# Optimization experiments

Hardware: AMD Instinct MI355X
Metric: run time of the kernel (lower is better)

## Reference

```python
import jax, jax.numpy as jnp
import numpy as np

NUM_HEADS = 16
ROPE_BASE = 10000.0
NEG_INF = float('-inf')


def _rotate_half_interleaved(x):
    # x: [..., d]; interleaved rotation: (-x2, x1) pairs
    x1 = x[..., ::2]
    x2 = x[..., 1::2]
    return jnp.stack((-x2, x1), axis=-1).reshape(x.shape)


def _rope_tables(seq_len, head_dim, dtype):
    inv_freq = 1.0 / (ROPE_BASE ** (jnp.arange(0, head_dim, 2, dtype=jnp.float32) / head_dim))
    pos = jnp.arange(seq_len, dtype=jnp.float32)
    freqs = pos[:, None] * inv_freq[None, :]          # [S, d/2]
    emb = jnp.concatenate((freqs, freqs), axis=-1)    # [S, d]  (HF-style concat, as in source)
    return jnp.cos(emb).astype(dtype), jnp.sin(emb).astype(dtype)


def setup_inputs() -> dict:
    key = jax.random.key(0)
    ks = jax.random.split(key, 4)
    B, S, H = 2, 2048, 2048
    scale = 0.02
    x = jax.random.normal(ks[0], (B, S, H), dtype=jnp.float32)
    qkv_w = jax.random.normal(ks[1], (3 * H, H), dtype=jnp.float32) * scale
    qkv_b = jnp.zeros((3 * H,), dtype=jnp.float32)
    out_w = jax.random.normal(ks[2], (H, H), dtype=jnp.float32) * scale
    out_b = jnp.zeros((H,), dtype=jnp.float32)
    attention_mask = jnp.ones((B, S), dtype=jnp.int32)
    return {"x": x, "attention_mask": attention_mask, "qkv_w": qkv_w,
            "qkv_b": qkv_b, "out_w": out_w, "out_b": out_b}


def reference(x, attention_mask, qkv_w, qkv_b, out_w, out_b):
    B, S, H = x.shape
    nh = NUM_HEADS
    hd = H // nh
    scale = hd ** -0.5

    qkv = x @ qkv_w.T + qkv_b                            # [B,S,3H]
    qkv = qkv.reshape(B, S, 3, nh, hd).transpose(2, 0, 3, 1, 4)  # [3,B,nh,S,hd]
    q, k, v = qkv[0], qkv[1], qkv[2]

    cos, sin = _rope_tables(S, hd, x.dtype)              # [S,hd]
    cos = cos[None, None, :, :]
    sin = sin[None, None, :, :]
    q = q * cos + _rotate_half_interleaved(q) * sin
    k = k * cos + _rotate_half_interleaved(k) * sin

    scores = jnp.einsum('bhqd,bhkd->bhqk', q, k) * scale  # [B,nh,S,S]
    causal = jnp.triu(jnp.ones((S, S), dtype=bool), k=1)
    scores = jnp.where(causal[None, None], NEG_INF, scores)
    key_mask = (attention_mask == 0)[:, None, None, :]    # [B,1,1,S]
    scores = jnp.where(key_mask, NEG_INF, scores)

    weights = jax.nn.softmax(scores, axis=-1)
    attn = jnp.einsum('bhqk,bhkd->bhqd', weights, v)       # [B,nh,S,hd]
    attn = attn.transpose(0, 2, 1, 3).reshape(B, S, H)
    return attn @ out_w.T + out_b
```

## Files before the change

### kernel.cpp

```cpp
#include <hip/hip_runtime.h>

typedef __bf16 bf16;
typedef __bf16 bf16x4 __attribute__((ext_vector_type(4)));
typedef __bf16 bf16x8 __attribute__((ext_vector_type(8)));
typedef float f32x4 __attribute__((ext_vector_type(4)));

#define MFMA_BF16(a, b, c) __builtin_amdgcn_mfma_f32_16x16x32_bf16(a, b, c, 0, 0, 0)

__device__ __forceinline__ void async16(const void* g, void* l) {
    __builtin_amdgcn_global_load_lds(
        (const __attribute__((address_space(1))) void*)g,
        (__attribute__((address_space(3))) void*)l,
        16, 0, 0);
}

__global__ void cvt8(const float* __restrict__ in, bf16* __restrict__ out, int n) {
    int i = (blockIdx.x * 256 + threadIdx.x) * 8;
    if (i >= n) return;
    float4 a = *(const float4*)(in + i);
    float4 b = *(const float4*)(in + i + 4);
    bf16x8 o;
    o[0] = (bf16)a.x; o[1] = (bf16)a.y; o[2] = (bf16)a.z; o[3] = (bf16)a.w;
    o[4] = (bf16)b.x; o[5] = (bf16)b.y; o[6] = (bf16)b.z; o[7] = (bf16)b.w;
    *(bf16x8*)(out + i) = o;
}

__global__ void tables_k(const int* __restrict__ am, float* __restrict__ cosT,
                         float* __restrict__ sinT, float* __restrict__ mbias) {
    int i = blockIdx.x * 256 + threadIdx.x;
    int s = i >> 7, d = i & 127, fi = d & 63;
    float inv = exp2f(-(float)fi * (13.287712379549449f / 64.0f));
    float ang = (float)s * inv;
    cosT[i] = cosf(ang);
    sinT[i] = sinf(ang);
    if (i < 2 * 2048) mbias[i] = (am[i] == 0) ? -1e30f : 0.0f;
}

template <int EPI>
__global__ void __launch_bounds__(256, 2)
gemm_bt(const bf16* __restrict__ A, const bf16* __restrict__ Bt,
        const float* __restrict__ bias, float* __restrict__ Cf,
        bf16* __restrict__ qb, bf16* __restrict__ kb, bf16* __restrict__ vtb,
        const float* __restrict__ cosT, const float* __restrict__ sinT,
        int M, int N, int K) {
    __shared__ __align__(16) bf16 sA[128 * 64];
    __shared__ __align__(16) bf16 sB[128 * 64];
    const int tid  = threadIdx.x;
    const int lane = tid & 63;
    const int quad = lane >> 4, l15 = lane & 15;
    const int wid = tid >> 6, wm = wid >> 1, wn = wid & 1;
    const int bm = blockIdx.x, bn = blockIdx.y;

    f32x4 acc[4][4];
#pragma unroll
    for (int i = 0; i < 4; i++)
#pragma unroll
        for (int j = 0; j < 4; j++)
#pragma unroll
            for (int c = 0; c < 4; c++) acc[i][j][c] = 0.0f;

    const int r0 = tid >> 3, x0 = tid & 7;
    const int g0 = x0 ^ (r0 & 7);
    const bf16* pa = A  + (size_t)(bm * 128 + r0) * K + g0 * 8;
    const bf16* pb = Bt + (size_t)(bn * 128 + r0) * K + g0 * 8;
    bf16* la = sA + tid * 8;
    bf16* lb = sB + tid * 8;
    const size_t gstep = (size_t)32 * K;

    for (int k0 = 0; k0 < K; k0 += 64) {
#pragma unroll
        for (int i = 0; i < 4; i++) {
            async16(pa + i * gstep, la + i * 2048);
            async16(pb + i * gstep, lb + i * 2048);
        }
        pa += 64; pb += 64;
        __syncthreads();
#pragma unroll
        for (int ks = 0; ks < 2; ks++) {
            bf16x8 af[4], bfr[4];
#pragma unroll
            for (int i = 0; i < 4; i++) {
                int r = wm * 64 + i * 16 + l15;
                int x = (ks * 4 + quad) ^ (r & 7);
                af[i] = *(const bf16x8*)(sA + r * 64 + x * 8);
            }
#pragma unroll
            for (int i = 0; i < 4; i++) {
                int r = wn * 64 + i * 16 + l15;
                int x = (ks * 4 + quad) ^ (r & 7);
                bfr[i] = *(const bf16x8*)(sB + r * 64 + x * 8);
            }
#pragma unroll
            for (int mi = 0; mi < 4; mi++)
#pragma unroll
                for (int ni = 0; ni < 4; ni++)
                    acc[mi][ni] = MFMA_BF16(af[mi], bfr[ni], acc[mi][ni]);
        }
        __syncthreads();
    }

    if (EPI == 0) {
#pragma unroll
        for (int mi = 0; mi < 4; mi++)
#pragma unroll
            for (int ni = 0; ni < 4; ni++) {
                int row0 = bm * 128 + wm * 64 + mi * 16 + quad * 4;
                int col  = bn * 128 + wn * 64 + ni * 16 + l15;
                float bv = bias[col];
#pragma unroll
                for (int r = 0; r < 4; r++)
                    Cf[(size_t)(row0 + r) * N + col] = acc[mi][ni][r] + bv;
            }
    } else {
#pragma unroll
        for (int mi = 0; mi < 4; mi++)
#pragma unroll
            for (int ni = 0; ni < 4; ni++) {
                int col   = bn * 128 + wn * 64 + ni * 16 + l15;
                int which = col >> 11;
                int hcol  = col & 2047;
                int h = hcol >> 7, d = hcol & 127;
                float bv = bias[col];
#pragma unroll
                for (int r = 0; r < 4; r++) {
                    int row = bm * 128 + wm * 64 + mi * 16 + quad * 4 + r;
                    int b = row >> 11, s = row & 2047;
                    float v  = acc[mi][ni][r] + bv;
                    float vp = __shfl_xor(v, 1, 64);
                    float ov = v;
                    if (which < 2) {
                        float c  = cosT[(s << 7) + d];
                        float sn = sinT[(s << 7) + d];
                        ov = v * c + ((d & 1) ? vp : -vp) * sn;
                    }
                    if (which == 0) ov *= 0.08838834764831845f;
                    size_t bh = (size_t)(b * 16 + h);
                    if (which == 0)      qb[(bh * 2048 + s) * 128 + d] = (bf16)ov;
                    else if (which == 1) kb[(bh * 2048 + s) * 128 + d] = (bf16)ov;
                    else                 vtb[(bh * 128 + d) * 2048 + s] = (bf16)ov;
                }
            }
    }
}

__global__ void __launch_bounds__(256, 4)
fattn(const bf16* __restrict__ Q, const bf16* __restrict__ Kg,
      const bf16* __restrict__ Vt, const float* __restrict__ mbias,
      bf16* __restrict__ O) {
    __shared__ __align__(16) bf16 sK[64 * 128];
    __shared__ __align__(16) bf16 sV[128 * 64];
    __shared__ __align__(16) bf16 sP[4 * 16 * 64];
    const int tid = threadIdx.x, lane = tid & 63, w = tid >> 6;
    const int quad = lane >> 4, l15 = lane & 15;
    const int qt = 31 - (int)blockIdx.x;
    const int bh = blockIdx.y;
    const int b = bh >> 4, h = bh & 15;
    const int rowbase = qt * 64 + w * 16;
    const int myq = rowbase + l15;

    const bf16* Qb  = Q  + (size_t)bh * 2048 * 128;
    const bf16* Kbh = Kg + (size_t)bh * 2048 * 128;
    const bf16* Vbh = Vt + (size_t)bh * 128 * 2048;
    const float* mbb = mbias + b * 2048;

    bf16x8 qf[4];
#pragma unroll
    for (int kq = 0; kq < 4; kq++)
        qf[kq] = *(const bf16x8*)(Qb + (size_t)myq * 128 + kq * 32 + quad * 8);

    f32x4 oacc[8];
#pragma unroll
    for (int ni = 0; ni < 8; ni++)
#pragma unroll
        for (int c = 0; c < 4; c++) oacc[ni][c] = 0.0f;
    float m_s = -3e38f, l_s = 0.0f;

    const int rk = tid >> 4, xk = tid & 15, gk = xk ^ (rk & 15);
    const int rv = tid >> 3, xv = tid & 7,  gv = xv ^ (rv & 7);
    const int nkt = qt + 1;

    for (int kt = 0; kt < nkt; kt++) {
        const int kb0 = kt * 64;
#pragma unroll
        for (int i = 0; i < 4; i++) {
            async16(Kbh + (size_t)(kb0 + rk + i * 16) * 128 + gk * 8, sK + (i * 256 + tid) * 8);
            async16(Vbh + (size_t)(rv + i * 32) * 2048 + kb0 + gv * 8, sV + (i * 256 + tid) * 8);
        }
        __syncthreads();

        f32x4 sacc[4];
#pragma unroll
        for (int nj = 0; nj < 4; nj++)
#pragma unroll
            for (int c = 0; c < 4; c++) sacc[nj][c] = 0.0f;
#pragma unroll
        for (int kq = 0; kq < 4; kq++) {
            bf16x8 kf[4];
#pragma unroll
            for (int nj = 0; nj < 4; nj++) {
                int r = nj * 16 + l15;
                int x = (kq * 4 + quad) ^ (r & 15);
                kf[nj] = *(const bf16x8*)(sK + r * 128 + x * 8);
            }
#pragma unroll
            for (int nj = 0; nj < 4; nj++)
                sacc[nj] = MFMA_BF16(kf[nj], qf[kq], sacc[nj]);
        }

        float pv[4][4];
#pragma unroll
        for (int nj = 0; nj < 4; nj++) {
            float4 mb4 = *(const float4*)(mbb + kb0 + nj * 16 + quad * 4);
#pragma unroll
            for (int r = 0; r < 4; r++) {
                int sk = kb0 + nj * 16 + quad * 4 + r;
                float val = sacc[nj][r] + ((const float*)&mb4)[r];
                pv[nj][r] = (sk > myq) ? -1e30f : val;
            }
        }

        float mx = -3e38f;
#pragma unroll
        for (int nj = 0; nj < 4; nj++)
#pragma unroll
            for (int r = 0; r < 4; r++) mx = fmaxf(mx, pv[nj][r]);
        mx = fmaxf(mx, __shfl_xor(mx, 16, 64));
        mx = fmaxf(mx, __shfl_xor(mx, 32, 64));
        float mnew  = fmaxf(m_s, mx);
        float alpha = __expf(m_s - mnew);
        float rs = 0.0f;
#pragma unroll
        for (int nj = 0; nj < 4; nj++)
#pragma unroll
            for (int r = 0; r < 4; r++) {
                float p = __expf(pv[nj][r] - mnew);
                pv[nj][r] = p;
                rs += p;
            }
        rs += __shfl_xor(rs, 16, 64);
        rs += __shfl_xor(rs, 32, 64);
        l_s = l_s * alpha + rs;
        m_s = mnew;
#pragma unroll
        for (int ni = 0; ni < 8; ni++) oacc[ni] *= alpha;

#pragma unroll
        for (int nj = 0; nj < 4; nj++) {
            int chunk = nj * 2 + (quad >> 1);
            int x = chunk ^ (l15 & 7);
            bf16* dst = sP + w * 1024 + l15 * 64 + x * 8 + (quad & 1) * 4;
#pragma unroll
            for (int r = 0; r < 4; r++) dst[r] = (bf16)pv[nj][r];
        }

#pragma unroll
        for (int kq2 = 0; kq2 < 2; kq2++) {
            int xp = (kq2 * 4 + quad) ^ (l15 & 7);
            bf16x8 pf = *(const bf16x8*)(sP + w * 1024 + l15 * 64 + xp * 8);
#pragma unroll
            for (int ni = 0; ni < 8; ni++) {
                int r = ni * 16 + l15;
                int x = (kq2 * 4 + quad) ^ (r & 7);
                bf16x8 vf = *(const bf16x8*)(sV + r * 64 + x * 8);
                oacc[ni] = MFMA_BF16(vf, pf, oacc[ni]);
            }
        }
        __syncthreads();
    }

    float inv = 1.0f / l_s;
    size_t base = ((size_t)(b * 2048 + myq)) * 2048 + h * 128;
#pragma unroll
    for (int ni = 0; ni < 8; ni++) {
        bf16x4 o4;
#pragma unroll
        for (int r = 0; r < 4; r++) o4[r] = (bf16)(oacc[ni][r] * inv);
        *(bf16x4*)(O + base + ni * 16 + quad * 4) = o4;
    }
}

extern "C" void kernel_launch(void* const* d_in, const int* in_sizes, int n_in,
                              void* d_out, int out_size, void* d_ws, size_t ws_size,
                              hipStream_t stream) {
    const float* x     = (const float*)d_in[0];
    const int*   am    = (const int*)d_in[1];
    const float* qkvw  = (const float*)d_in[2];
    const float* qkvb  = (const float*)d_in[3];
    const float* outw  = (const float*)d_in[4];
    const float* outb  = (const float*)d_in[5];
    float* out = (float*)d_out;

    char* ws = (char*)d_ws;
    bf16*  xb    = (bf16*)(ws);
    bf16*  wqkv  = (bf16*)(ws + (16ull << 20));
    bf16*  wout  = (bf16*)(ws + (40ull << 20));
    bf16*  qb    = (bf16*)(ws + (48ull << 20));
    bf16*  kb    = (bf16*)(ws + (64ull << 20));
    bf16*  vtb   = (bf16*)(ws + (80ull << 20));
    bf16*  attn  = (bf16*)(ws + (96ull << 20));
    float* cosT  = (float*)(ws + (112ull << 20));
    float* sinT  = (float*)(ws + (113ull << 20));
    float* mbias = (float*)(ws + (114ull << 20));

    cvt8<<<4096, 256, 0, stream>>>(x, xb, 4096 * 2048);
    cvt8<<<6144, 256, 0, stream>>>(qkvw, wqkv, 6144 * 2048);
    cvt8<<<2048, 256, 0, stream>>>(outw, wout, 2048 * 2048);
    tables_k<<<1024, 256, 0, stream>>>(am, cosT, sinT, mbias);

    gemm_bt<1><<<dim3(32, 48), 256, 0, stream>>>(
        xb, wqkv, qkvb, nullptr, qb, kb, vtb, cosT, sinT, 4096, 6144, 2048);

    fattn<<<dim3(32, 32), 256, 0, stream>>>(qb, kb, vtb, mbias, attn);

    gemm_bt<0><<<dim3(32, 16), 256, 0, stream>>>(
        attn, wout, outb, out, nullptr, nullptr, nullptr, nullptr, nullptr,
        4096, 2048, 2048);
}
```

Baseline: 429.5 us.

## Use 32x32 MFMA with 128-row query tiles and balanced causal tile ordering in attention

The flash-attention kernel now uses 32x32x16 bf16 MFMA instructions, and each wave handles 32 query rows, so a block covers 128 queries instead of 64. Every K/V tile loaded into shared memory is reused across twice as many queries, and the softmax row reductions need one fewer cross-lane shuffle. Query tiles are interleaved from both ends of the causal triangle to balance work across blocks. The cost is a larger register footprint (occupancy hint lowered to 2), half as many blocks, and a larger P scratch buffer in shared memory.

New measurement: 413.4 us. 3.7% less time.

```diff
diff --git a/kernel.cpp b/kernel.cpp
--- a/kernel.cpp
+++ b/kernel.cpp
@@ -4,8 +4,10 @@
 typedef __bf16 bf16x4 __attribute__((ext_vector_type(4)));
 typedef __bf16 bf16x8 __attribute__((ext_vector_type(8)));
 typedef float f32x4 __attribute__((ext_vector_type(4)));
+typedef float f32x16 __attribute__((ext_vector_type(16)));
 
 #define MFMA_BF16(a, b, c) __builtin_amdgcn_mfma_f32_16x16x32_bf16(a, b, c, 0, 0, 0)
+#define MFMA32(a, b, c)    __builtin_amdgcn_mfma_f32_32x32x16_bf16(a, b, c, 0, 0, 0)
 
 __device__ __forceinline__ void async16(const void* g, void* l) {
     __builtin_amdgcn_global_load_lds(
@@ -143,41 +145,41 @@
     }
 }
 
-__global__ void __launch_bounds__(256, 4)
+__global__ void __launch_bounds__(256, 2)
 fattn(const bf16* __restrict__ Q, const bf16* __restrict__ Kg,
       const bf16* __restrict__ Vt, const float* __restrict__ mbias,
       bf16* __restrict__ O) {
     __shared__ __align__(16) bf16 sK[64 * 128];
     __shared__ __align__(16) bf16 sV[128 * 64];
-    __shared__ __align__(16) bf16 sP[4 * 16 * 64];
+    __shared__ __align__(16) bf16 sP[4 * 32 * 64];
     const int tid = threadIdx.x, lane = tid & 63, w = tid >> 6;
-    const int quad = lane >> 4, l15 = lane & 15;
-    const int qt = 31 - (int)blockIdx.x;
-    const int bh = blockIdx.y;
-    const int b = bh >> 4, h = bh & 15;
-    const int rowbase = qt * 64 + w * 16;
-    const int myq = rowbase + l15;
+    const int l31 = lane & 31, half = lane >> 5;
+    const int bx = (int)blockIdx.x;
+    const int qt = (bx & 1) ? 15 - (bx >> 1) : (bx >> 1);
+    const int bh = blockIdx.y, b = bh >> 4, hh = bh & 15;
+    const int myq = qt * 128 + w * 32 + l31;
 
     const bf16* Qb  = Q  + (size_t)bh * 2048 * 128;
     const bf16* Kbh = Kg + (size_t)bh * 2048 * 128;
     const bf16* Vbh = Vt + (size_t)bh * 128 * 2048;
     const float* mbb = mbias + b * 2048;
-
-    bf16x8 qf[4];
-#pragma unroll
-    for (int kq = 0; kq < 4; kq++)
-        qf[kq] = *(const bf16x8*)(Qb + (size_t)myq * 128 + kq * 32 + quad * 8);
-
-    f32x4 oacc[8];
-#pragma unroll
-    for (int ni = 0; ni < 8; ni++)
-#pragma unroll
-        for (int c = 0; c < 4; c++) oacc[ni][c] = 0.0f;
+    bf16* sPw = sP + w * 2048;
+
+    bf16x8 qf[8];
+#pragma unroll
+    for (int kq = 0; kq < 8; kq++)
+        qf[kq] = *(const bf16x8*)(Qb + (size_t)myq * 128 + kq * 16 + half * 8);
+
+    f32x16 oacc[4];
+#pragma unroll
+    for (int dt = 0; dt < 4; dt++)
+#pragma unroll
+        for (int c = 0; c < 16; c++) oacc[dt][c] = 0.0f;
     float m_s = -3e38f, l_s = 0.0f;
 
     const int rk = tid >> 4, xk = tid & 15, gk = xk ^ (rk & 15);
     const int rv = tid >> 3, xv = tid & 7,  gv = xv ^ (rv & 7);
-    const int nkt = qt + 1;
+    const int nkt = 2 * qt + 2;
 
     for (int kt = 0; kt < nkt; kt++) {
         const int kb0 = kt * 64;
@@ -188,95 +190,96 @@
         }
         __syncthreads();
 
-        f32x4 sacc[4];
-#pragma unroll
-        for (int nj = 0; nj < 4; nj++)
-#pragma unroll
-            for (int c = 0; c < 4; c++) sacc[nj][c] = 0.0f;
-#pragma unroll
-        for (int kq = 0; kq < 4; kq++) {
-            bf16x8 kf[4];
-#pragma unroll
-            for (int nj = 0; nj < 4; nj++) {
-                int r = nj * 16 + l15;
-                int x = (kq * 4 + quad) ^ (r & 15);
-                kf[nj] = *(const bf16x8*)(sK + r * 128 + x * 8);
-            }
-#pragma unroll
-            for (int nj = 0; nj < 4; nj++)
-                sacc[nj] = MFMA_BF16(kf[nj], qf[kq], sacc[nj]);
-        }
-
-        float pv[4][4];
-#pragma unroll
-        for (int nj = 0; nj < 4; nj++) {
-            float4 mb4 = *(const float4*)(mbb + kb0 + nj * 16 + quad * 4);
-#pragma unroll
-            for (int r = 0; r < 4; r++) {
-                int sk = kb0 + nj * 16 + quad * 4 + r;
-                float val = sacc[nj][r] + ((const float*)&mb4)[r];
-                pv[nj][r] = (sk > myq) ? -1e30f : val;
-            }
-        }
-
+        f32x16 sacc[2];
+#pragma unroll
+        for (int t = 0; t < 2; t++)
+#pragma unroll
+            for (int c = 0; c < 16; c++) sacc[t][c] = 0.0f;
+#pragma unroll
+        for (int kq = 0; kq < 8; kq++) {
+#pragma unroll
+            for (int t = 0; t < 2; t++) {
+                int row = t * 32 + l31;
+                int x = (kq * 2 + half) ^ (row & 15);
+                bf16x8 kf = *(const bf16x8*)(sK + row * 128 + x * 8);
+                sacc[t] = MFMA32(kf, qf[kq], sacc[t]);
+            }
+        }
+
+        float ps[2][16];
         float mx = -3e38f;
 #pragma unroll
-        for (int nj = 0; nj < 4; nj++)
-#pragma unroll
-            for (int r = 0; r < 4; r++) mx = fmaxf(mx, pv[nj][r]);
-        mx = fmaxf(mx, __shfl_xor(mx, 16, 64));
+        for (int t = 0; t < 2; t++)
+#pragma unroll
+            for (int g = 0; g < 4; g++) {
+                float4 mb4 = *(const float4*)(mbb + kb0 + t * 32 + 8 * g + 4 * half);
+#pragma unroll
+                for (int r2 = 0; r2 < 4; r2++) {
+                    int sk = kb0 + t * 32 + 8 * g + 4 * half + r2;
+                    float v = sacc[t][g * 4 + r2] + ((const float*)&mb4)[r2];
+                    v = (sk > myq) ? -1e30f : v;
+                    ps[t][g * 4 + r2] = v;
+                    mx = fmaxf(mx, v);
+                }
+            }
+
         mx = fmaxf(mx, __shfl_xor(mx, 32, 64));
         float mnew  = fmaxf(m_s, mx);
         float alpha = __expf(m_s - mnew);
         float rs = 0.0f;
 #pragma unroll
-        for (int nj = 0; nj < 4; nj++)
-#pragma unroll
-            for (int r = 0; r < 4; r++) {
-                float p = __expf(pv[nj][r] - mnew);
-                pv[nj][r] = p;
+        for (int t = 0; t < 2; t++)
+#pragma unroll
+            for (int c = 0; c < 16; c++) {
+                float p = __expf(ps[t][c] - mnew);
+                ps[t][c] = p;
                 rs += p;
             }
-        rs += __shfl_xor(rs, 16, 64);
         rs += __shfl_xor(rs, 32, 64);
         l_s = l_s * alpha + rs;
         m_s = mnew;
 #pragma unroll
-        for (int ni = 0; ni < 8; ni++) oacc[ni] *= alpha;
-
-#pragma unroll
-        for (int nj = 0; nj < 4; nj++) {
-            int chunk = nj * 2 + (quad >> 1);
-            int x = chunk ^ (l15 & 7);
-            bf16* dst = sP + w * 1024 + l15 * 64 + x * 8 + (quad & 1) * 4;
-#pragma unroll
-            for (int r = 0; r < 4; r++) dst[r] = (bf16)pv[nj][r];
-        }
-
-#pragma unroll
-        for (int kq2 = 0; kq2 < 2; kq2++) {
-            int xp = (kq2 * 4 + quad) ^ (l15 & 7);
-            bf16x8 pf = *(const bf16x8*)(sP + w * 1024 + l15 * 64 + xp * 8);
-#pragma unroll
-            for (int ni = 0; ni < 8; ni++) {
-                int r = ni * 16 + l15;
-                int x = (kq2 * 4 + quad) ^ (r & 7);
-                bf16x8 vf = *(const bf16x8*)(sV + r * 64 + x * 8);
-                oacc[ni] = MFMA_BF16(vf, pf, oacc[ni]);
+        for (int dt = 0; dt < 4; dt++) oacc[dt] *= alpha;
+
+#pragma unroll
+        for (int t = 0; t < 2; t++)
+#pragma unroll
+            for (int g = 0; g < 4; g++) {
+                int c = t * 4 + g;
+                int x = c ^ (l31 & 7);
+                bf16x4 p4;
+#pragma unroll
+                for (int r2 = 0; r2 < 4; r2++) p4[r2] = (bf16)ps[t][g * 4 + r2];
+                *(bf16x4*)(sPw + l31 * 64 + x * 8 + half * 4) = p4;
+            }
+
+#pragma unroll
+        for (int kq2 = 0; kq2 < 4; kq2++) {
+            int cp = kq2 * 2 + half;
+            int xp = cp ^ (l31 & 7);
+            bf16x8 pf = *(const bf16x8*)(sPw + l31 * 64 + xp * 8);
+#pragma unroll
+            for (int dt = 0; dt < 4; dt++) {
+                int row = dt * 32 + l31;
+                int xv2 = cp ^ (row & 7);
+                bf16x8 vf = *(const bf16x8*)(sV + row * 64 + xv2 * 8);
+                oacc[dt] = MFMA32(vf, pf, oacc[dt]);
             }
         }
         __syncthreads();
     }
 
     float inv = 1.0f / l_s;
-    size_t base = ((size_t)(b * 2048 + myq)) * 2048 + h * 128;
-#pragma unroll
-    for (int ni = 0; ni < 8; ni++) {
-        bf16x4 o4;
-#pragma unroll
-        for (int r = 0; r < 4; r++) o4[r] = (bf16)(oacc[ni][r] * inv);
-        *(bf16x4*)(O + base + ni * 16 + quad * 4) = o4;
-    }
+    size_t base = ((size_t)(b * 2048 + myq)) * 2048 + hh * 128;
+#pragma unroll
+    for (int dt = 0; dt < 4; dt++)
+#pragma unroll
+        for (int g = 0; g < 4; g++) {
+            bf16x4 o4;
+#pragma unroll
+            for (int r2 = 0; r2 < 4; r2++) o4[r2] = (bf16)(oacc[dt][g * 4 + r2] * inv);
+            *(bf16x4*)(O + base + dt * 32 + 8 * g + 4 * half) = o4;
+        }
 }
 
 extern "C" void kernel_launch(void* const* d_in, const int* in_sizes, int n_in,
@@ -310,7 +313,7 @@
     gemm_bt<1><<<dim3(32, 48), 256, 0, stream>>>(
         xb, wqkv, qkvb, nullptr, qb, kb, vtb, cosT, sinT, 4096, 6144, 2048);
 
-    fattn<<<dim3(32, 32), 256, 0, stream>>>(qb, kb, vtb, mbias, attn);
+    fattn<<<dim3(16, 32), 256, 0, stream>>>(qb, kb, vtb, mbias, attn);
 
     gemm_bt<0><<<dim3(32, 16), 256, 0, stream>>>(
         attn, wout, outb, out, nullptr, nullptr, nullptr, nullptr, nullptr,
```
